# Kernel optimization log

Hardware: AMD Instinct MI355X
Metric: run time of the kernel (lower is better)

The kernel has to match this reference:

```python
import jax, jax.numpy as jnp
import numpy as np

D_MODEL = 1024
NHEAD = 16
HEAD_DIM = D_MODEL // NHEAD


def setup_inputs() -> dict:
    key = jax.random.key(0)
    ks = jax.random.split(key, 9)
    s = 0.02
    x = jax.random.normal(ks[0], (2, 2048, D_MODEL), dtype=jnp.float32)
    Wq = jax.random.normal(ks[1], (D_MODEL, D_MODEL), dtype=jnp.float32) * s
    bq = jnp.zeros((D_MODEL,), jnp.float32)
    Wk = jax.random.normal(ks[2], (D_MODEL, D_MODEL), dtype=jnp.float32) * s
    bk = jnp.zeros((D_MODEL,), jnp.float32)
    Wv = jax.random.normal(ks[3], (D_MODEL, D_MODEL), dtype=jnp.float32) * s
    bv = jnp.zeros((D_MODEL,), jnp.float32)
    Wo = jax.random.normal(ks[4], (D_MODEL, D_MODEL), dtype=jnp.float32) * s
    bo = jnp.zeros((D_MODEL,), jnp.float32)
    return {"x": x, "Wq": Wq, "bq": bq, "Wk": Wk, "bk": bk,
            "Wv": Wv, "bv": bv, "Wo": Wo, "bo": bo}


def _rope(x, sin, cos):
    # x: [B, L, H, Dh]; rotate-half as in the torch module
    half = x.shape[-1] // 2
    x1, x2 = x[..., :half], x[..., half:]
    rotated = jnp.concatenate([-x2, x1], axis=-1)
    return x * cos + rotated * sin


def reference(x, Wq, bq, Wk, bk, Wv, bv, Wo, bo):
    B, L, D = x.shape
    H, Dh = NHEAD, HEAD_DIM
    q = (x @ Wq.T + bq).reshape(B, L, H, Dh)
    k = (x @ Wk.T + bk).reshape(B, L, H, Dh)
    v = (x @ Wv.T + bv).reshape(B, L, H, Dh)

    inv_freq = 1.0 / (10000.0 ** (jnp.arange(0, Dh, 2, dtype=jnp.float32) / Dh))
    t = jnp.arange(L, dtype=jnp.float32)
    freqs = jnp.einsum('i,j->ij', t, inv_freq)          # [L, Dh/2]
    emb = jnp.concatenate([freqs, freqs], axis=-1)      # [L, Dh]
    cos = jnp.cos(emb)[None, :, None, :]
    sin = jnp.sin(emb)[None, :, None, :]

    q = _rope(q, sin, cos)
    k = _rope(k, sin, cos)

    # [B, H, L, L]
    scores = jnp.einsum('bqhd,bkhd->bhqk', q, k) / jnp.sqrt(jnp.float32(Dh))
    attn = jax.nn.softmax(scores, axis=-1)
    # dropout in eval mode = identity (p given as 0.0)
    out = jnp.einsum('bhqk,bkhd->bqhd', attn, v).reshape(B, L, D)
    return out @ Wo.T + bo
```

## Files before the change

### kernel.cpp

```cpp
#include <hip/hip_runtime.h>
#include <math.h>

#define D_MODEL 1024
#define NHEAD 16
#define HEAD_DIM 64
#define L_SEQ 2048
#define BATCH 2
#define M_ROWS 4096
#define SC_Q 0.18033688011112042f

typedef __attribute__((ext_vector_type(8))) short short8;
typedef __attribute__((ext_vector_type(4))) float floatx4;
typedef __attribute__((ext_vector_type(2))) __fp16 half2_t;
typedef __attribute__((ext_vector_type(4))) __fp16 half4_t;
typedef __attribute__((ext_vector_type(8))) __fp16 half8_t;

#if __has_builtin(__builtin_amdgcn_exp2f)
#define EXP2F(x) __builtin_amdgcn_exp2f(x)
#else
#define EXP2F(x) exp2f(x)
#endif

__device__ inline unsigned f2bf_u(float x) {
    unsigned u = __float_as_uint(x);
    return (u + 0x7fffu + ((u >> 16) & 1u)) >> 16;
}

__device__ inline void gl_lds16(const void* g, void* l) {
    __builtin_amdgcn_global_load_lds((const __attribute__((address_space(1))) void*)g,
                                     (__attribute__((address_space(3))) void*)l, 16, 0, 0);
}

__device__ inline void permlane16_swap(unsigned& a, unsigned& b) {
#if __has_builtin(__builtin_amdgcn_permlane16_swap)
    auto r = __builtin_amdgcn_permlane16_swap(a, b, false, false);
    a = r[0];
    b = r[1];
#else
    asm("v_permlane16_swap_b32 %0, %1" : "+v"(a), "+v"(b));
#endif
}

__global__ __launch_bounds__(256) void cvt_all(
    const float* __restrict__ x,  const float* __restrict__ wq,
    const float* __restrict__ wk, const float* __restrict__ wv,
    const float* __restrict__ wo,
    unsigned short* __restrict__ xb,  unsigned short* __restrict__ wqb,
    unsigned short* __restrict__ wkb, unsigned short* __restrict__ wvb,
    unsigned short* __restrict__ wob, float* __restrict__ rt) {
    if (blockIdx.y == 5) {
        for (int idx = blockIdx.x * 256 + threadIdx.x; idx < L_SEQ * 16;
             idx += gridDim.x * 256) {
            int l = idx >> 4, f = idx & 15;
            float if0 = (float)pow(10000.0, -(double)f / 32.0);
            float if1 = (float)pow(10000.0, -(double)(f + 16) / 32.0);
            float s0, c0, s1, c1;
            sincosf((float)l * if0, &s0, &c0);
            sincosf((float)l * if1, &s1, &c1);
            float4 v = {c0, c1, s0, s1};
            *(float4*)(rt + (size_t)idx * 4) = v;
        }
        return;
    }
    const float* s; unsigned short* d; int n;
    switch (blockIdx.y) {
        case 0:  s = x;  d = xb;  n = M_ROWS * D_MODEL; break;
        case 1:  s = wq; d = wqb; n = D_MODEL * D_MODEL; break;
        case 2:  s = wk; d = wkb; n = D_MODEL * D_MODEL; break;
        case 3:  s = wv; d = wvb; n = D_MODEL * D_MODEL; break;
        default: s = wo; d = wob; n = D_MODEL * D_MODEL; break;
    }
    int stride = gridDim.x * 256 * 4;
    for (int i = (blockIdx.x * 256 + threadIdx.x) * 4; i < n; i += stride) {
        float4 v = *(const float4*)(s + i);
        ushort4 o;
        o.x = (unsigned short)f2bf_u(v.x);
        o.y = (unsigned short)f2bf_u(v.y);
        o.z = (unsigned short)f2bf_u(v.z);
        o.w = (unsigned short)f2bf_u(v.w);
        *(ushort4*)(d + i) = o;
    }
}

__global__ __launch_bounds__(256) void gemm_qkv(
    const unsigned short* __restrict__ xb,
    const unsigned short* __restrict__ wqb, const unsigned short* __restrict__ wkb,
    const unsigned short* __restrict__ wvb,
    const float* __restrict__ bq, const float* __restrict__ bk,
    const float* __restrict__ bv, const float* __restrict__ rt,
    unsigned short* __restrict__ qo, unsigned short* __restrict__ ko,
    unsigned short* __restrict__ vo) {
    __shared__ __align__(16) unsigned short As[128 * 32];
    __shared__ __align__(16) unsigned short Bs[128 * 32];

    const int K = D_MODEL;
    const int tid = threadIdx.x;
    const int lane = tid & 63;
    const int w = tid >> 6;
    const int wm = (w & 1) * 64;
    const int wn = (w >> 1) * 64;
    const int m0 = blockIdx.x * 128;
    const int n0 = blockIdx.y * 128;

    const unsigned short* Wsel; const float* bsel;
    unsigned short* osel; int mode; float oscale;
    if (blockIdx.z == 0)      { Wsel = wqb; bsel = bq; osel = qo; mode = 1; oscale = SC_Q; }
    else if (blockIdx.z == 1) { Wsel = wkb; bsel = bk; osel = ko; mode = 1; oscale = 1.0f; }
    else                      { Wsel = wvb; bsel = bv; osel = vo; mode = 2; oscale = 1.0f; }

    floatx4 acc[4][4];
#pragma unroll
    for (int i = 0; i < 4; ++i)
#pragma unroll
        for (int j = 0; j < 4; ++j) acc[i][j] = (floatx4){0.f, 0.f, 0.f, 0.f};

    const int sr = lane >> 2;
    const int ss = lane & 3;
    const unsigned short* Ag = xb + (size_t)m0 * K;
    const unsigned short* Bg = Wsel + (size_t)n0 * K;

    for (int k0 = 0; k0 < K; k0 += 32) {
        __syncthreads();
#pragma unroll
        for (int t = 0; t < 2; ++t) {
            int R0 = t * 64 + w * 16;
            int r = R0 + sr;
            int c = ss ^ ((r >> 1) & 3);
            gl_lds16(Ag + (size_t)r * K + k0 + c * 8, (void*)(As + R0 * 32));
            gl_lds16(Bg + (size_t)r * K + k0 + c * 8, (void*)(Bs + R0 * 32));
        }
        __syncthreads();

        short8 af[4], bf[4];
#pragma unroll
        for (int mt = 0; mt < 4; ++mt) {
            int ar = wm + mt * 16 + (lane & 15);
            int slot = (lane >> 4) ^ ((ar >> 1) & 3);
            af[mt] = *(const short8*)(As + ar * 32 + slot * 8);
        }
#pragma unroll
        for (int nt = 0; nt < 4; ++nt) {
            int br = wn + nt * 16 + (lane & 15);
            int slot = (lane >> 4) ^ ((br >> 1) & 3);
            bf[nt] = *(const short8*)(Bs + br * 32 + slot * 8);
        }
#pragma unroll
        for (int mt = 0; mt < 4; ++mt)
#pragma unroll
            for (int nt = 0; nt < 4; ++nt)
                acc[mt][nt] = __builtin_amdgcn_mfma_f32_16x16x32_bf16(
                    af[mt], bf[nt], acc[mt][nt], 0, 0, 0);
    }

#pragma unroll
    for (int nt = 0; nt < 4; ++nt) {
        float bn = bsel[n0 + wn + nt * 16 + (lane & 15)];
#pragma unroll
        for (int mt = 0; mt < 4; ++mt)
#pragma unroll
            for (int i = 0; i < 4; ++i) acc[mt][nt][i] += bn;
    }

    const int h = (n0 + wn) >> 6;

    if (mode == 1) {
#pragma unroll
        for (int mt = 0; mt < 4; ++mt)
#pragma unroll
            for (int i = 0; i < 4; ++i) {
                int m = m0 + wm + mt * 16 + (lane >> 4) * 4 + i;
                int b = m >> 11, l = m & (L_SEQ - 1);
                float4 tc = *(const float4*)(rt + ((size_t)(l * 16 + (lane & 15)) << 2));
#pragma unroll
                for (int nt = 0; nt < 4; ++nt) {
                    int dh = nt * 16 + (lane & 15);
                    float partner = acc[mt][nt ^ 2][i];
                    float rot = (nt < 2) ? -partner : partner;
                    float c = (nt & 1) ? tc.y : tc.x;
                    float s = (nt & 1) ? tc.w : tc.z;
                    float val = (acc[mt][nt][i] * c + rot * s) * oscale;
                    size_t idx = (((size_t)(b * NHEAD + h)) * L_SEQ + l) * HEAD_DIM + dh;
                    osel[idx] = (unsigned short)f2bf_u(val);
                }
            }
    } else {
#pragma unroll
        for (int mt = 0; mt < 4; ++mt)
#pragma unroll
            for (int ih = 0; ih < 4; ih += 2) {
                int m = m0 + wm + mt * 16 + (lane >> 4) * 4 + ih;
                int b = m >> 11, l = m & (L_SEQ - 1);
#pragma unroll
                for (int nt = 0; nt < 4; ++nt) {
                    int dh = nt * 16 + (lane & 15);
                    union { half2_t h; unsigned u; } cv;
                    cv.h = __builtin_amdgcn_cvt_pkrtz(acc[mt][nt][ih], acc[mt][nt][ih + 1]);
                    size_t idx = (((size_t)(b * NHEAD + h)) * HEAD_DIM + dh) * L_SEQ + l;
                    *(unsigned*)(vo + idx) = cv.u;
                }
            }
    }
}

__global__ __launch_bounds__(256) void gemm_out(
    const unsigned short* __restrict__ A, const unsigned short* __restrict__ Wb,
    const float* __restrict__ bias, float* __restrict__ out) {
    __shared__ __align__(16) unsigned short As[64 * 32];
    __shared__ __align__(16) unsigned short Bs[128 * 32];

    const int K = D_MODEL;
    const int tid = threadIdx.x;
    const int lane = tid & 63;
    const int w = tid >> 6;
    const int wm = (w & 1) * 32;
    const int wn = (w >> 1) * 64;
    const int m0 = blockIdx.x * 64;
    const int n0 = blockIdx.y * 128;

    floatx4 acc[2][4];
#pragma unroll
    for (int i = 0; i < 2; ++i)
#pragma unroll
        for (int j = 0; j < 4; ++j) acc[i][j] = (floatx4){0.f, 0.f, 0.f, 0.f};

    const int sr = lane >> 2;
    const int ss = lane & 3;
    const unsigned short* Ag = A + (size_t)m0 * K;
    const unsigned short* Bg = Wb + (size_t)n0 * K;

    for (int k0 = 0; k0 < K; k0 += 32) {
        __syncthreads();
        {
            int r = w * 16 + sr;
            int c = ss ^ ((r >> 1) & 3);
            gl_lds16(Ag + (size_t)r * K + k0 + c * 8, (void*)(As + (w * 16) * 32));
        }
#pragma unroll
        for (int t = 0; t < 2; ++t) {
            int R0 = t * 64 + w * 16;
            int r = R0 + sr;
            int c = ss ^ ((r >> 1) & 3);
            gl_lds16(Bg + (size_t)r * K + k0 + c * 8, (void*)(Bs + R0 * 32));
        }
        __syncthreads();

        short8 af[2], bf[4];
#pragma unroll
        for (int mt = 0; mt < 2; ++mt) {
            int ar = wm + mt * 16 + (lane & 15);
            int slot = (lane >> 4) ^ ((ar >> 1) & 3);
            af[mt] = *(const short8*)(As + ar * 32 + slot * 8);
        }
#pragma unroll
        for (int nt = 0; nt < 4; ++nt) {
            int br = wn + nt * 16 + (lane & 15);
            int slot = (lane >> 4) ^ ((br >> 1) & 3);
            bf[nt] = *(const short8*)(Bs + br * 32 + slot * 8);
        }
#pragma unroll
        for (int mt = 0; mt < 2; ++mt)
#pragma unroll
            for (int nt = 0; nt < 4; ++nt)
                acc[mt][nt] = __builtin_amdgcn_mfma_f32_16x16x32_bf16(
                    af[mt], bf[nt], acc[mt][nt], 0, 0, 0);
    }

#pragma unroll
    for (int nt = 0; nt < 4; ++nt) {
        int n = n0 + wn + nt * 16 + (lane & 15);
        float bn = bias[n];
#pragma unroll
        for (int mt = 0; mt < 2; ++mt)
#pragma unroll
            for (int i = 0; i < 4; ++i) {
                int m = m0 + wm + mt * 16 + (lane >> 4) * 4 + i;
                out[(size_t)m * D_MODEL + n] = acc[mt][nt][i] + bn;
            }
    }
}

__global__ __launch_bounds__(256, 4) void attn_mfma(
    const unsigned short* __restrict__ q, const unsigned short* __restrict__ k,
    const unsigned short* __restrict__ vt,
    unsigned short* __restrict__ ao) {
    __shared__ __align__(16) unsigned short Ks[128 * 64];
    __shared__ __align__(16) unsigned short Vs[64 * 128];

    const int tid = threadIdx.x;
    const int lane = tid & 63;
    const int w = tid >> 6;
    const int quad = lane >> 4;
    const int ln = lane & 15;

    const int GX = L_SEQ / 128;
    int lin = blockIdx.y * GX + blockIdx.x;
    lin = (lin & 7) * 64 + (lin >> 3);
    const int q0 = (lin & (GX - 1)) * 128;
    const int bh = lin >> 4;

    const unsigned short* qb = q + (size_t)bh * L_SEQ * HEAD_DIM;
    const unsigned short* kb = k + (size_t)bh * L_SEQ * HEAD_DIM;
    const unsigned short* vb = vt + (size_t)bh * HEAD_DIM * L_SEQ;

    short8 qf[2][2];
#pragma unroll
    for (int ntq = 0; ntq < 2; ++ntq)
#pragma unroll
        for (int ks = 0; ks < 2; ++ks)
            qf[ntq][ks] = *(const short8*)(
                qb + (size_t)(q0 + w * 32 + ntq * 16 + ln) * HEAD_DIM
                + ks * 32 + quad * 8);

    floatx4 o[2][4];
    floatx4 ls[2];
#pragma unroll
    for (int ntq = 0; ntq < 2; ++ntq) {
        ls[ntq] = (floatx4){0.f, 0.f, 0.f, 0.f};
#pragma unroll
        for (int j = 0; j < 4; ++j) o[ntq][j] = (floatx4){0.f, 0.f, 0.f, 0.f};
    }

    half8_t ones8;
#pragma unroll
    for (int j = 0; j < 8; ++j) ones8[j] = (__fp16)1.0f;

    const int srk = lane >> 3;
    const int ssk = lane & 7;
    const int srv = lane >> 4;
    const int ssv = lane & 15;
    const int pb = ((quad & 1) << 1) | (quad >> 1);

    for (int t = 0; t < L_SEQ / 128; ++t) {
        int kv0 = t * 128;
        __syncthreads();
#pragma unroll
        for (int tt = 0; tt < 4; ++tt) {
            {
                int R0 = tt * 32 + w * 8;
                int r = R0 + srk;
                int c = ssk ^ (r & 7);
                gl_lds16(kb + (size_t)(kv0 + r) * HEAD_DIM + c * 8, (void*)(Ks + R0 * 64));
            }
            {
                int R0 = tt * 16 + w * 4;
                int r = R0 + srv;
                int c = ssv ^ (r & 15);
                gl_lds16(vb + (size_t)r * L_SEQ + kv0 + c * 8, (void*)(Vs + R0 * 128));
            }
        }
        __syncthreads();

#pragma unroll
        for (int mt2 = 0; mt2 < 4; ++mt2) {
            floatx4 s[2][2];
#pragma unroll
            for (int c = 0; c < 2; ++c) {
                int ar = mt2 * 32 + c * 16 + ln;
                short8 kf0 = *(const short8*)(Ks + ar * 64 + ((quad) ^ (ar & 7)) * 8);
                short8 kf1 = *(const short8*)(Ks + ar * 64 + ((4 + quad) ^ (ar & 7)) * 8);

                floatx4 t0 = (floatx4){0.f, 0.f, 0.f, 0.f};
                floatx4 t1 = (floatx4){0.f, 0.f, 0.f, 0.f};
                t0 = __builtin_amdgcn_mfma_f32_16x16x32_bf16(kf0, qf[0][0], t0, 0, 0, 0);
                t0 = __builtin_amdgcn_mfma_f32_16x16x32_bf16(kf1, qf[0][1], t0, 0, 0, 0);
                t1 = __builtin_amdgcn_mfma_f32_16x16x32_bf16(kf0, qf[1][0], t1, 0, 0, 0);
                t1 = __builtin_amdgcn_mfma_f32_16x16x32_bf16(kf1, qf[1][1], t1, 0, 0, 0);
                s[c][0] = t0;
                s[c][1] = t1;
            }

            half8_t vf[4];
#pragma unroll
            for (int ntd = 0; ntd < 4; ++ntd) {
                int row = ntd * 16 + ln;
                int slot = (mt2 * 4 + pb) ^ (row & 15);
                vf[ntd] = *(const half8_t*)(Vs + row * 128 + slot * 8);
            }

#pragma unroll
            for (int tq = 0; tq < 2; ++tq) {
                union { half2_t h; unsigned u; } c0l, c0h, c1l, c1h;
                c0l.h = __builtin_amdgcn_cvt_pkrtz(EXP2F(s[0][tq][0]), EXP2F(s[0][tq][1]));
                c0h.h = __builtin_amdgcn_cvt_pkrtz(EXP2F(s[0][tq][2]), EXP2F(s[0][tq][3]));
                c1l.h = __builtin_amdgcn_cvt_pkrtz(EXP2F(s[1][tq][0]), EXP2F(s[1][tq][1]));
                c1h.h = __builtin_amdgcn_cvt_pkrtz(EXP2F(s[1][tq][2]), EXP2F(s[1][tq][3]));
                unsigned a0 = c0l.u, b0 = c1l.u;
                unsigned a1 = c0h.u, b1 = c1h.u;
                permlane16_swap(a0, b0);
                permlane16_swap(a1, b1);
                union { half8_t h8; unsigned u[4]; } af;
                af.u[0] = a0; af.u[1] = a1; af.u[2] = b0; af.u[3] = b1;

                ls[tq] = __builtin_amdgcn_mfma_f32_16x16x32_f16(af.h8, ones8, ls[tq], 0, 0, 0);
#pragma unroll
                for (int ntd = 0; ntd < 4; ++ntd)
                    o[tq][ntd] = __builtin_amdgcn_mfma_f32_16x16x32_f16(
                        af.h8, vf[ntd], o[tq][ntd], 0, 0, 0);
            }
        }
    }

    const int b = bh >> 4, h = bh & (NHEAD - 1);
#pragma unroll
    for (int ntq = 0; ntq < 2; ++ntq)
#pragma unroll
        for (int i = 0; i < 4; ++i) {
            int l = q0 + w * 32 + ntq * 16 + quad * 4 + i;
            float inv = 1.0f / ls[ntq][i];
#pragma unroll
            for (int ntd = 0; ntd < 4; ++ntd) {
                int dh = ntd * 16 + ln;
                size_t idx = ((size_t)b * L_SEQ + l) * D_MODEL + h * HEAD_DIM + dh;
                ao[idx] = (unsigned short)f2bf_u(o[ntq][ntd][i] * inv);
            }
        }
}

extern "C" void kernel_launch(void* const* d_in, const int* in_sizes, int n_in,
                              void* d_out, int out_size, void* d_ws, size_t ws_size,
                              hipStream_t stream) {
    const float* x  = (const float*)d_in[0];
    const float* Wq = (const float*)d_in[1];
    const float* bq = (const float*)d_in[2];
    const float* Wk = (const float*)d_in[3];
    const float* bk = (const float*)d_in[4];
    const float* Wv = (const float*)d_in[5];
    const float* bv = (const float*)d_in[6];
    const float* Wo = (const float*)d_in[7];
    const float* bo = (const float*)d_in[8];
    float* outp = (float*)d_out;

    const size_t XE = (size_t)M_ROWS * D_MODEL;
    const size_t WE = (size_t)D_MODEL * D_MODEL;
    unsigned short* wqb = (unsigned short*)d_ws;
    unsigned short* wkb = wqb + WE;
    unsigned short* wvb = wkb + WE;
    unsigned short* wob = wvb + WE;
    unsigned short* qbf = wob + WE;
    unsigned short* kbf = qbf + XE;
    unsigned short* vtb = kbf + XE;
    unsigned short* xb  = vtb + XE;
    unsigned short* aob = xb;
    float* rt    = (float*)(xb + XE);

    cvt_all<<<dim3(1024, 6), 256, 0, stream>>>(x, Wq, Wk, Wv, Wo,
                                               xb, wqb, wkb, wvb, wob, rt);

    gemm_qkv<<<dim3(M_ROWS / 128, D_MODEL / 128, 3), 256, 0, stream>>>(
        xb, wqb, wkb, wvb, bq, bk, bv, rt, qbf, kbf, vtb);

    attn_mfma<<<dim3(L_SEQ / 128, BATCH * NHEAD), 256, 0, stream>>>(
        qbf, kbf, vtb, aob);

    gemm_out<<<dim3(M_ROWS / 64, D_MODEL / 128), 256, 0, stream>>>(aob, wob, bo, outp);
}
```

Before: 188.9 us.

## Double-buffer K/V tiles in attention kernel to overlap loads with compute

Adds a second LDS buffer for K and V tiles in the attention kernel and stages tile t+1 while computing tile t, which halves the barriers per tile and hides global-to-LDS latency. LDS use doubles from 32KB to 64KB per block, which may lower occupancy against the launch bound of 4 blocks per CU. It depends on the async gl_lds16 loads completing before the barrier.

```diff
diff --git a/kernel.cpp b/kernel.cpp
--- a/kernel.cpp
+++ b/kernel.cpp
@@ -283,8 +283,10 @@
     const unsigned short* __restrict__ q, const unsigned short* __restrict__ k,
     const unsigned short* __restrict__ vt,
     unsigned short* __restrict__ ao) {
-    __shared__ __align__(16) unsigned short Ks[128 * 64];
-    __shared__ __align__(16) unsigned short Vs[64 * 128];
+    __shared__ __align__(16) unsigned short KsA[128 * 64];
+    __shared__ __align__(16) unsigned short VsA[64 * 128];
+    __shared__ __align__(16) unsigned short KsB[128 * 64];
+    __shared__ __align__(16) unsigned short VsB[64 * 128];
 
     const int tid = threadIdx.x;
     const int lane = tid & 63;
@@ -330,34 +332,36 @@
     const int ssv = lane & 15;
     const int pb = ((quad & 1) << 1) | (quad >> 1);
 
-    for (int t = 0; t < L_SEQ / 128; ++t) {
-        int kv0 = t * 128;
-        __syncthreads();
-#pragma unroll
-        for (int tt = 0; tt < 4; ++tt) {
-            {
-                int R0 = tt * 32 + w * 8;
-                int r = R0 + srk;
-                int c = ssk ^ (r & 7);
-                gl_lds16(kb + (size_t)(kv0 + r) * HEAD_DIM + c * 8, (void*)(Ks + R0 * 64));
-            }
-            {
-                int R0 = tt * 16 + w * 4;
-                int r = R0 + srv;
-                int c = ssv ^ (r & 15);
-                gl_lds16(vb + (size_t)r * L_SEQ + kv0 + c * 8, (void*)(Vs + R0 * 128));
-            }
-        }
-        __syncthreads();
-
+#define STAGE_TILE(KsX, VsX, kv0)                                             \
+    do {                                                                      \
+        _Pragma("unroll")                                                     \
+        for (int tt = 0; tt < 4; ++tt) {                                      \
+            {                         \
+                int R0 = tt * 32 + w * 8;                                     \
+                int r = R0 + srk;                                             \
+                int c = ssk ^ (r & 7);                                        \
+                gl_lds16(kb + (size_t)((kv0) + r) * HEAD_DIM + c * 8,         \
+                         (void*)(KsX + R0 * 64));                             \
+            }                                                                 \
+            {                         \
+                int R0 = tt * 16 + w * 4;                                     \
+                int r = R0 + srv;                                             \
+                int c = ssv ^ (r & 15);                                       \
+                gl_lds16(vb + (size_t)r * L_SEQ + (kv0) + c * 8,              \
+                         (void*)(VsX + R0 * 128));                            \
+            }                                                                 \
+        }                                                                     \
+    } while (0)
+
+    auto compute_tile = [&](const unsigned short* KsP, const unsigned short* VsP) {
 #pragma unroll
         for (int mt2 = 0; mt2 < 4; ++mt2) {
             floatx4 s[2][2];
 #pragma unroll
             for (int c = 0; c < 2; ++c) {
                 int ar = mt2 * 32 + c * 16 + ln;
-                short8 kf0 = *(const short8*)(Ks + ar * 64 + ((quad) ^ (ar & 7)) * 8);
-                short8 kf1 = *(const short8*)(Ks + ar * 64 + ((4 + quad) ^ (ar & 7)) * 8);
+                short8 kf0 = *(const short8*)(KsP + ar * 64 + ((quad) ^ (ar & 7)) * 8);
+                short8 kf1 = *(const short8*)(KsP + ar * 64 + ((4 + quad) ^ (ar & 7)) * 8);
 
                 floatx4 t0 = (floatx4){0.f, 0.f, 0.f, 0.f};
                 floatx4 t1 = (floatx4){0.f, 0.f, 0.f, 0.f};
@@ -374,7 +378,7 @@
             for (int ntd = 0; ntd < 4; ++ntd) {
                 int row = ntd * 16 + ln;
                 int slot = (mt2 * 4 + pb) ^ (row & 15);
-                vf[ntd] = *(const half8_t*)(Vs + row * 128 + slot * 8);
+                vf[ntd] = *(const half8_t*)(VsP + row * 128 + slot * 8);
             }
 
 #pragma unroll
@@ -398,7 +402,20 @@
                         af.h8, vf[ntd], o[tq][ntd], 0, 0, 0);
             }
         }
-    }
+    };
+
+    const int NT = L_SEQ / 128;
+    STAGE_TILE(KsA, VsA, 0);
+    __syncthreads();
+    for (int t = 0; t < NT; t += 2) {
+        STAGE_TILE(KsB, VsB, (t + 1) * 128);
+        compute_tile(KsA, VsA);
+        __syncthreads();
+        if (t + 2 < NT) STAGE_TILE(KsA, VsA, (t + 2) * 128);
+        compute_tile(KsB, VsB);
+        __syncthreads();
+    }
+#undef STAGE_TILE
 
     const int b = bh >> 4, h = bh & (NHEAD - 1);
 #pragma unroll
```

Result: faster. 185.2 us (-2.0%).

## Load K and V fragments directly from global memory, dropping LDS staging

Applied to the files above, without the earlier changes.

The attention kernel no longer stages K and V tiles into shared memory with async global-to-LDS copies and barriers. Each wave now reads its MFMA operand fragments straight from global memory, relying on L1/L2 caching for reuse across the four waves of a block. This removes the two __syncthreads per KV tile and the LDS footprint, which may allow more occupancy. In exchange, each of the four waves loads the same K/V data separately, and latency that was previously hidden by the bulk copies is now exposed.

```diff
diff --git a/kernel.cpp b/kernel.cpp
--- a/kernel.cpp
+++ b/kernel.cpp
@@ -283,9 +283,6 @@
     const unsigned short* __restrict__ q, const unsigned short* __restrict__ k,
     const unsigned short* __restrict__ vt,
     unsigned short* __restrict__ ao) {
-    __shared__ __align__(16) unsigned short Ks[128 * 64];
-    __shared__ __align__(16) unsigned short Vs[64 * 128];
-
     const int tid = threadIdx.x;
     const int lane = tid & 63;
     const int w = tid >> 6;
@@ -324,40 +321,22 @@
 #pragma unroll
     for (int j = 0; j < 8; ++j) ones8[j] = (__fp16)1.0f;
 
-    const int srk = lane >> 3;
-    const int ssk = lane & 7;
-    const int srv = lane >> 4;
-    const int ssv = lane & 15;
     const int pb = ((quad & 1) << 1) | (quad >> 1);
 
+    const unsigned short* kL = kb + (size_t)ln * HEAD_DIM + quad * 8;
+    const unsigned short* vL = vb + (size_t)ln * L_SEQ + pb * 8;
+
     for (int t = 0; t < L_SEQ / 128; ++t) {
-        int kv0 = t * 128;
-        __syncthreads();
-#pragma unroll
-        for (int tt = 0; tt < 4; ++tt) {
-            {
-                int R0 = tt * 32 + w * 8;
-                int r = R0 + srk;
-                int c = ssk ^ (r & 7);
-                gl_lds16(kb + (size_t)(kv0 + r) * HEAD_DIM + c * 8, (void*)(Ks + R0 * 64));
-            }
-            {
-                int R0 = tt * 16 + w * 4;
-                int r = R0 + srv;
-                int c = ssv ^ (r & 15);
-                gl_lds16(vb + (size_t)r * L_SEQ + kv0 + c * 8, (void*)(Vs + R0 * 128));
-            }
-        }
-        __syncthreads();
+        const int kv0 = t * 128;
 
 #pragma unroll
         for (int mt2 = 0; mt2 < 4; ++mt2) {
             floatx4 s[2][2];
 #pragma unroll
             for (int c = 0; c < 2; ++c) {
-                int ar = mt2 * 32 + c * 16 + ln;
-                short8 kf0 = *(const short8*)(Ks + ar * 64 + ((quad) ^ (ar & 7)) * 8);
-                short8 kf1 = *(const short8*)(Ks + ar * 64 + ((4 + quad) ^ (ar & 7)) * 8);
+                const unsigned short* kr = kL + (size_t)(kv0 + mt2 * 32 + c * 16) * HEAD_DIM;
+                short8 kf0 = *(const short8*)(kr);
+                short8 kf1 = *(const short8*)(kr + 32);
 
                 floatx4 t0 = (floatx4){0.f, 0.f, 0.f, 0.f};
                 floatx4 t1 = (floatx4){0.f, 0.f, 0.f, 0.f};
@@ -371,11 +350,9 @@
 
             half8_t vf[4];
 #pragma unroll
-            for (int ntd = 0; ntd < 4; ++ntd) {
-                int row = ntd * 16 + ln;
-                int slot = (mt2 * 4 + pb) ^ (row & 15);
-                vf[ntd] = *(const half8_t*)(Vs + row * 128 + slot * 8);
-            }
+            for (int ntd = 0; ntd < 4; ++ntd)
+                vf[ntd] = *(const half8_t*)(vL + (size_t)(ntd * 16) * L_SEQ
+                                            + kv0 + mt2 * 32);
 
 #pragma unroll
             for (int tq = 0; tq < 2; ++tq) {
```

Result: slower. 260.1 us (+37.7%).

## Load V fragments directly from global into registers with double-buffering

Applied to the files above, without the earlier changes.

Drops the LDS staging buffer for V. Each lane now reads its V fragments straight from global memory, and those loads are double-buffered in registers across the four sub-tiles so they overlap with the QK and PV MFMA work. This removes the LDS writes and reads for V and halves shared memory per block, which may allow higher occupancy. In exchange, the four waves in a block each fetch V redundantly from global or L2 using 16-byte strided accesses, and register pressure goes up.

```diff
diff --git a/kernel.cpp b/kernel.cpp
--- a/kernel.cpp
+++ b/kernel.cpp
@@ -284,7 +284,6 @@
     const unsigned short* __restrict__ vt,
     unsigned short* __restrict__ ao) {
     __shared__ __align__(16) unsigned short Ks[128 * 64];
-    __shared__ __align__(16) unsigned short Vs[64 * 128];
 
     const int tid = threadIdx.x;
     const int lane = tid & 63;
@@ -326,32 +325,34 @@
 
     const int srk = lane >> 3;
     const int ssk = lane & 7;
-    const int srv = lane >> 4;
-    const int ssv = lane & 15;
     const int pb = ((quad & 1) << 1) | (quad >> 1);
 
+    const unsigned short* vP0 = vb + (size_t)ln * L_SEQ + pb * 8;
+    const unsigned short* vP1 = vP0 + (size_t)16 * L_SEQ;
+    const unsigned short* vP2 = vP0 + (size_t)32 * L_SEQ;
+    const unsigned short* vP3 = vP0 + (size_t)48 * L_SEQ;
+
     for (int t = 0; t < L_SEQ / 128; ++t) {
-        int kv0 = t * 128;
+        const int kv0 = t * 128;
         __syncthreads();
 #pragma unroll
         for (int tt = 0; tt < 4; ++tt) {
-            {
-                int R0 = tt * 32 + w * 8;
-                int r = R0 + srk;
-                int c = ssk ^ (r & 7);
-                gl_lds16(kb + (size_t)(kv0 + r) * HEAD_DIM + c * 8, (void*)(Ks + R0 * 64));
-            }
-            {
-                int R0 = tt * 16 + w * 4;
-                int r = R0 + srv;
-                int c = ssv ^ (r & 15);
-                gl_lds16(vb + (size_t)r * L_SEQ + kv0 + c * 8, (void*)(Vs + R0 * 128));
-            }
-        }
-        __syncthreads();
-
-#pragma unroll
-        for (int mt2 = 0; mt2 < 4; ++mt2) {
+            int R0 = tt * 32 + w * 8;
+            int r = R0 + srk;
+            int c = ssk ^ (r & 7);
+            gl_lds16(kb + (size_t)(kv0 + r) * HEAD_DIM + c * 8, (void*)(Ks + R0 * 64));
+        }
+        __syncthreads();
+
+        half8_t vA[4], vB[4];
+        auto loadV = [&](half8_t (&dst)[4], int mt2) {
+            dst[0] = *(const half8_t*)(vP0 + kv0 + mt2 * 32);
+            dst[1] = *(const half8_t*)(vP1 + kv0 + mt2 * 32);
+            dst[2] = *(const half8_t*)(vP2 + kv0 + mt2 * 32);
+            dst[3] = *(const half8_t*)(vP3 + kv0 + mt2 * 32);
+        };
+
+        auto do_mt2 = [&](int mt2, half8_t (&vf)[4]) {
             floatx4 s[2][2];
 #pragma unroll
             for (int c = 0; c < 2; ++c) {
@@ -367,14 +368,6 @@
                 t1 = __builtin_amdgcn_mfma_f32_16x16x32_bf16(kf1, qf[1][1], t1, 0, 0, 0);
                 s[c][0] = t0;
                 s[c][1] = t1;
-            }
-
-            half8_t vf[4];
-#pragma unroll
-            for (int ntd = 0; ntd < 4; ++ntd) {
-                int row = ntd * 16 + ln;
-                int slot = (mt2 * 4 + pb) ^ (row & 15);
-                vf[ntd] = *(const half8_t*)(Vs + row * 128 + slot * 8);
             }
 
 #pragma unroll
@@ -397,7 +390,16 @@
                     o[tq][ntd] = __builtin_amdgcn_mfma_f32_16x16x32_f16(
                         af.h8, vf[ntd], o[tq][ntd], 0, 0, 0);
             }
-        }
+        };
+
+        loadV(vA, 0);
+        loadV(vB, 1);
+        do_mt2(0, vA);
+        loadV(vA, 2);
+        do_mt2(1, vB);
+        loadV(vB, 3);
+        do_mt2(2, vA);
+        do_mt2(3, vB);
     }
 
     const int b = bh >> 4, h = bh & (NHEAD - 1);
```

After: 229.3 us. +21.4%, slower.
